# Kernel optimization log

Hardware: AMD Instinct MI355X
Metric: run time of the kernel (lower is better)

Reference implementation:

```python
import jax, jax.numpy as jnp
import numpy as np

TOPK = 8
NUM_EXPERT_GROUP = 8
TOPK_GROUP = 4
ROUTED_SCALING_FACTOR = 2.5

NUM_TOKENS = 131072
NUM_EXPERTS = 256


def setup_inputs() -> dict:
    key = jax.random.key(0)
    k1, k2 = jax.random.split(key)
    router_logits = jax.random.normal(k1, (NUM_TOKENS, NUM_EXPERTS), dtype=jnp.float32)
    correction_bias = jax.random.normal(k2, (NUM_EXPERTS,), dtype=jnp.float32)
    return {"router_logits": router_logits, "correction_bias": correction_bias}


def reference(router_logits, correction_bias):
    # Biased grouped top-k router (DeepSeek-V3 style), faithful to TopK.__call__
    logits = router_logits.astype(jnp.float32)          # [T, E]
    T, E = logits.shape
    G = NUM_EXPERT_GROUP
    experts_per_group = E // G

    scores_for_choice = logits + correction_bias[None, :]            # [T, E]
    scores_grouped = scores_for_choice.reshape(T, G, experts_per_group)
    # group score = sum of top-2 biased scores in each group
    group_scores = jnp.sum(jax.lax.top_k(scores_grouped, k=2)[0], axis=-1)  # [T, G]
    group_idx = jax.lax.top_k(group_scores, k=TOPK_GROUP)[1]                 # [T, KG]
    group_mask = jnp.clip(jax.nn.one_hot(group_idx, G).sum(axis=1), 0, 1)    # [T, G]
    score_mask = jnp.broadcast_to(group_mask[:, :, None], (T, G, experts_per_group)).reshape(T, E)
    tmp_scores = jnp.where(score_mask.astype(bool), scores_for_choice, float("-inf"))
    topk_ids = jax.lax.top_k(tmp_scores, k=TOPK)[1]                          # [T, K]
    # weights are gathered from the UNbiased logits
    topk_weights = jnp.take_along_axis(logits, topk_ids, axis=1)             # [T, K]
    # renormalize + routed scaling factor
    topk_weights = topk_weights / jnp.sum(topk_weights, axis=-1, keepdims=True)
    topk_weights = topk_weights * ROUTED_SCALING_FACTOR
    return topk_weights.astype(jnp.float32), topk_ids
```

## Files before the change

kernel.cpp:

```cpp
#include <hip/hip_runtime.h>
#include <stdint.h>
#include <math.h>

static constexpr int TOPK   = 8;
static constexpr int TOPKG  = 4;
static constexpr int NEXP   = 256;
static constexpr float RSF  = 2.5f;

static constexpr int DPP_QX1 = 0xB1;
static constexpr int DPP_QX2 = 0x4E;
static constexpr int DPP_HM  = 0x141;
static constexpr int DPP_MIR = 0x140;
static constexpr int DPP_B15 = 0x142;
static constexpr int DPP_B31 = 0x143;

template <int CTRL>
__device__ __forceinline__ float dppmov(float x) {
    int xi = __float_as_int(x);
    return __int_as_float(__builtin_amdgcn_update_dpp(xi, xi, CTRL, 0xF, 0xF, false));
}

__device__ __forceinline__ void cas(float& ax, float& ay, int& ix, int& iy) {
    bool p   = ax < ay;
    float hi = fmaxf(ax, ay), lo = fminf(ax, ay);
    int   nx = p ? iy : ix,   ny = p ? ix : iy;
    ax = hi; ay = lo; ix = nx; iy = ny;
}

__global__ __launch_bounds__(256) void router_kernel(
    const float* __restrict__ logits,
    const float* __restrict__ bias,
    float* __restrict__ out_w,
    float* __restrict__ out_id,
    int T)
{
    const int lane  = threadIdx.x & 63;
    const int token = blockIdx.x * (blockDim.x >> 6) + (threadIdx.x >> 6);
    if (token >= T) return;

    const float* row = logits + (size_t)token * NEXP;
    float4 v = ((const float4*)row)[lane];
    float4 b = ((const float4*)bias)[lane];

    float s0 = v.x + b.x;
    float s1 = v.y + b.y;
    float s2 = v.z + b.z;
    float s3 = v.w + b.w;

    float hi01 = fmaxf(s0, s1), lo01 = fminf(s0, s1);
    float hi23 = fmaxf(s2, s3), lo23 = fminf(s2, s3);
    float m1 = fmaxf(hi01, hi23);
    float m2 = fmaxf(fminf(hi01, hi23), fmaxf(lo01, lo23));
    {
        float o1 = dppmov<DPP_QX1>(m1), o2 = dppmov<DPP_QX1>(m2);
        float n1 = fmaxf(m1, o1);
        float n2 = fmaxf(fminf(m1, o1), fmaxf(m2, o2));
        m1 = n1; m2 = n2;
    }
    {
        float o1 = dppmov<DPP_QX2>(m1), o2 = dppmov<DPP_QX2>(m2);
        float n1 = fmaxf(m1, o1);
        float n2 = fmaxf(fminf(m1, o1), fmaxf(m2, o2));
        m1 = n1; m2 = n2;
    }
    {
        float o1 = dppmov<DPP_HM>(m1), o2 = dppmov<DPP_HM>(m2);
        float n1 = fmaxf(m1, o1);
        float n2 = fmaxf(fminf(m1, o1), fmaxf(m2, o2));
        m1 = n1; m2 = n2;
    }
    const float gscore = m1 + m2;

    const int g = lane >> 3;
    const int j = lane & 7;
    float gj = __shfl(gscore, j << 3, 64);
    bool beats = (gj > gscore) || (gj == gscore && j < g);
    uint64_t bal = __ballot(beats);
    int rank = __popcll(bal & (0xFFull << (g << 3)));
    const bool sel = (rank < TOPKG);

    const float NEG = -INFINITY;
    float a0 = sel ? s0 : NEG;
    float a1 = sel ? s1 : NEG;
    float a2 = sel ? s2 : NEG;
    float a3 = sel ? s3 : NEG;
    const int ebase = lane << 2;
    int i0 = ebase, i1 = ebase + 1, i2 = ebase + 2, i3 = ebase + 3;
    cas(a0, a1, i0, i1);
    cas(a2, a3, i2, i3);
    cas(a0, a2, i0, i2);
    cas(a1, a3, i1, i3);
    cas(a1, a2, i1, i2);
    uint32_t ipack = (uint32_t)i0 | ((uint32_t)i1 << 8) |
                     ((uint32_t)i2 << 16) | ((uint32_t)i3 << 24);
    int i0cur = i0;

    int   myid = 0;
    float myw  = 0.f;
    #pragma unroll
    for (int r = 0; r < TOPK; ++r) {
        float x = a0;
        x = fmaxf(x, dppmov<DPP_QX1>(x));
        x = fmaxf(x, dppmov<DPP_QX2>(x));
        x = fmaxf(x, dppmov<DPP_HM >(x));
        x = fmaxf(x, dppmov<DPP_MIR>(x));
        x = fmaxf(x, dppmov<DPP_B15>(x));
        x = fmaxf(x, dppmov<DPP_B31>(x));
        const float smax = __int_as_float(
            __builtin_amdgcn_readlane(__float_as_int(x), 63));

        uint64_t wb  = __ballot(a0 == smax);
        const int wl = __ffsll((unsigned long long)wb) - 1;
        const int idx = __builtin_amdgcn_readlane(i0cur, wl);

        const bool mine = (lane == r);
        myid = mine ? idx  : myid;
        myw  = mine ? smax : myw;

        const bool win = (lane == wl);
        a0 = win ? a1  : a0;
        a1 = win ? a2  : a1;
        a2 = win ? a3  : a2;
        a3 = win ? NEG : a3;
        ipack = win ? (ipack >> 8) : ipack;
        i0cur = (int)(ipack & 255u);
    }

    float bi = 0.f;
    if (lane < TOPK) bi = bias[myid];
    float w = myw - bi;

    float t = w;
    t += dppmov<DPP_QX1>(t);
    t += dppmov<DPP_QX2>(t);
    t += dppmov<DPP_HM >(t);

    if (lane < TOPK) {
        out_w [(size_t)token * TOPK + lane] = w / t * RSF;
        out_id[(size_t)token * TOPK + lane] = (float)myid;
    }
}

extern "C" void kernel_launch(void* const* d_in, const int* in_sizes, int n_in,
                              void* d_out, int out_size, void* d_ws, size_t ws_size,
                              hipStream_t stream) {
    const float* logits = (const float*)d_in[0];
    const float* bias   = (const float*)d_in[1];
    const int T = in_sizes[0] / NEXP;
    float* out = (float*)d_out;
    float* out_w  = out;
    float* out_id = out + (size_t)T * TOPK;

    const int waves_per_block = 256 / 64;
    const int blocks = (T + waves_per_block - 1) / waves_per_block;
    router_kernel<<<blocks, 256, 0, stream>>>(logits, bias, out_w, out_id, T);
}
```

Before: 218.5 us.

## Use sortable uint keys and cached per-row maxima in top-k selection

Biased scores become order-preserving uint32 keys, so comparisons are integer max/select. The top-k loop keeps four cached row maxima (one per 16-lane row) and, after each pick, recomputes only the winner's row with a 4-step DPP reduction instead of a full 6-step wave reduction. The final weights are re-read from the logits row rather than subtracting bias from the stored score. Each round still pays a full row reduction plus a readlane, and re-reading the row adds a global load that will likely hit cache.

```diff
diff --git a/kernel.cpp b/kernel.cpp
--- a/kernel.cpp
+++ b/kernel.cpp
@@ -2,28 +2,35 @@
 #include <stdint.h>
 #include <math.h>
 
-static constexpr int TOPK   = 8;
-static constexpr int TOPKG  = 4;
-static constexpr int NEXP   = 256;
-static constexpr float RSF  = 2.5f;
+static constexpr int TOPK  = 8;
+static constexpr int TOPKG = 4;
+static constexpr int NEXP  = 256;
+static constexpr float RSF = 2.5f;
 
 static constexpr int DPP_QX1 = 0xB1;
 static constexpr int DPP_QX2 = 0x4E;
 static constexpr int DPP_HM  = 0x141;
 static constexpr int DPP_MIR = 0x140;
-static constexpr int DPP_B15 = 0x142;
-static constexpr int DPP_B31 = 0x143;
 
 template <int CTRL>
-__device__ __forceinline__ float dppmov(float x) {
+__device__ __forceinline__ float dppmov_f(float x) {
     int xi = __float_as_int(x);
     return __int_as_float(__builtin_amdgcn_update_dpp(xi, xi, CTRL, 0xF, 0xF, false));
 }
+template <int CTRL>
+__device__ __forceinline__ uint32_t dppmov_u(uint32_t x) {
+    return (uint32_t)__builtin_amdgcn_update_dpp((int)x, (int)x, CTRL, 0xF, 0xF, false);
+}
 
-__device__ __forceinline__ void cas(float& ax, float& ay, int& ix, int& iy) {
-    bool p   = ax < ay;
-    float hi = fmaxf(ax, ay), lo = fminf(ax, ay);
-    int   nx = p ? iy : ix,   ny = p ? ix : iy;
+__device__ __forceinline__ uint32_t f2sort(float f) {
+    uint32_t u = __float_as_uint(f);
+    return u ^ ((uint32_t)((int32_t)u >> 31) | 0x80000000u);
+}
+
+__device__ __forceinline__ void cas(uint32_t& ax, uint32_t& ay, int& ix, int& iy) {
+    bool p      = ax < ay;
+    uint32_t hi = p ? ay : ax, lo = p ? ax : ay;
+    int nx      = p ? iy : ix,  ny = p ? ix : iy;
     ax = hi; ay = lo; ix = nx; iy = ny;
 }
 
@@ -52,19 +59,19 @@
     float m1 = fmaxf(hi01, hi23);
     float m2 = fmaxf(fminf(hi01, hi23), fmaxf(lo01, lo23));
     {
-        float o1 = dppmov<DPP_QX1>(m1), o2 = dppmov<DPP_QX1>(m2);
+        float o1 = dppmov_f<DPP_QX1>(m1), o2 = dppmov_f<DPP_QX1>(m2);
         float n1 = fmaxf(m1, o1);
         float n2 = fmaxf(fminf(m1, o1), fmaxf(m2, o2));
         m1 = n1; m2 = n2;
     }
     {
-        float o1 = dppmov<DPP_QX2>(m1), o2 = dppmov<DPP_QX2>(m2);
+        float o1 = dppmov_f<DPP_QX2>(m1), o2 = dppmov_f<DPP_QX2>(m2);
         float n1 = fmaxf(m1, o1);
         float n2 = fmaxf(fminf(m1, o1), fmaxf(m2, o2));
         m1 = n1; m2 = n2;
     }
     {
-        float o1 = dppmov<DPP_HM>(m1), o2 = dppmov<DPP_HM>(m2);
+        float o1 = dppmov_f<DPP_HM>(m1), o2 = dppmov_f<DPP_HM>(m2);
         float n1 = fmaxf(m1, o1);
         float n2 = fmaxf(fminf(m1, o1), fmaxf(m2, o2));
         m1 = n1; m2 = n2;
@@ -75,15 +82,14 @@
     const int j = lane & 7;
     float gj = __shfl(gscore, j << 3, 64);
     bool beats = (gj > gscore) || (gj == gscore && j < g);
-    uint64_t bal = __ballot(beats);
-    int rank = __popcll(bal & (0xFFull << (g << 3)));
+    uint64_t balg = __ballot(beats);
+    int rank = __popcll(balg & (0xFFull << (g << 3)));
     const bool sel = (rank < TOPKG);
 
-    const float NEG = -INFINITY;
-    float a0 = sel ? s0 : NEG;
-    float a1 = sel ? s1 : NEG;
-    float a2 = sel ? s2 : NEG;
-    float a3 = sel ? s3 : NEG;
+    uint32_t a0 = sel ? f2sort(s0) : 0u;
+    uint32_t a1 = sel ? f2sort(s1) : 0u;
+    uint32_t a2 = sel ? f2sort(s2) : 0u;
+    uint32_t a3 = sel ? f2sort(s3) : 0u;
     const int ebase = lane << 2;
     int i0 = ebase, i1 = ebase + 1, i2 = ebase + 2, i3 = ebase + 3;
     cas(a0, a1, i0, i1);
@@ -93,47 +99,54 @@
     cas(a1, a2, i1, i2);
     uint32_t ipack = (uint32_t)i0 | ((uint32_t)i1 << 8) |
                      ((uint32_t)i2 << 16) | ((uint32_t)i3 << 24);
-    int i0cur = i0;
 
-    int   myid = 0;
-    float myw  = 0.f;
+    uint32_t bm = a0;
+    bm = max(bm, dppmov_u<DPP_QX1>(bm));
+    bm = max(bm, dppmov_u<DPP_QX2>(bm));
+    bm = max(bm, dppmov_u<DPP_HM >(bm));
+    bm = max(bm, dppmov_u<DPP_MIR>(bm));
+    uint32_t rm0 = (uint32_t)__builtin_amdgcn_readlane((int)bm,  0);
+    uint32_t rm1 = (uint32_t)__builtin_amdgcn_readlane((int)bm, 16);
+    uint32_t rm2 = (uint32_t)__builtin_amdgcn_readlane((int)bm, 32);
+    uint32_t rm3 = (uint32_t)__builtin_amdgcn_readlane((int)bm, 48);
+
+    int myid = 0;
     #pragma unroll
     for (int r = 0; r < TOPK; ++r) {
-        float x = a0;
-        x = fmaxf(x, dppmov<DPP_QX1>(x));
-        x = fmaxf(x, dppmov<DPP_QX2>(x));
-        x = fmaxf(x, dppmov<DPP_HM >(x));
-        x = fmaxf(x, dppmov<DPP_MIR>(x));
-        x = fmaxf(x, dppmov<DPP_B15>(x));
-        x = fmaxf(x, dppmov<DPP_B31>(x));
-        const float smax = __int_as_float(
-            __builtin_amdgcn_readlane(__float_as_int(x), 63));
+        const uint32_t smax = max(max(rm0, rm1), max(rm2, rm3));
 
-        uint64_t wb  = __ballot(a0 == smax);
-        const int wl = __ffsll((unsigned long long)wb) - 1;
-        const int idx = __builtin_amdgcn_readlane(i0cur, wl);
+        const uint64_t bal = __ballot(a0 == smax);
+        const int wl  = __ffsll((unsigned long long)bal) - 1;
+        const int idx = __builtin_amdgcn_readlane((int)ipack, wl) & 255;
 
-        const bool mine = (lane == r);
-        myid = mine ? idx  : myid;
-        myw  = mine ? smax : myw;
+        myid = (lane == r) ? idx : myid;
 
         const bool win = (lane == wl);
-        a0 = win ? a1  : a0;
-        a1 = win ? a2  : a1;
-        a2 = win ? a3  : a2;
-        a3 = win ? NEG : a3;
+        a0 = win ? a1 : a0;
+        a1 = win ? a2 : a1;
+        a2 = win ? a3 : a2;
+        a3 = win ? 0u : a3;
         ipack = win ? (ipack >> 8) : ipack;
-        i0cur = (int)(ipack & 255u);
+
+        uint32_t nb = a0;
+        nb = max(nb, dppmov_u<DPP_QX1>(nb));
+        nb = max(nb, dppmov_u<DPP_QX2>(nb));
+        nb = max(nb, dppmov_u<DPP_HM >(nb));
+        nb = max(nb, dppmov_u<DPP_MIR>(nb));
+        const uint32_t nbm = (uint32_t)__builtin_amdgcn_readlane((int)nb, wl);
+        const int blk = wl >> 4;
+        rm0 = (blk == 0) ? nbm : rm0;
+        rm1 = (blk == 1) ? nbm : rm1;
+        rm2 = (blk == 2) ? nbm : rm2;
+        rm3 = (blk == 3) ? nbm : rm3;
     }
 
-    float bi = 0.f;
-    if (lane < TOPK) bi = bias[myid];
-    float w = myw - bi;
-
+    float w = 0.f;
+    if (lane < TOPK) w = row[myid];
     float t = w;
-    t += dppmov<DPP_QX1>(t);
-    t += dppmov<DPP_QX2>(t);
-    t += dppmov<DPP_HM >(t);
+    t += dppmov_f<DPP_QX1>(t);
+    t += dppmov_f<DPP_QX2>(t);
+    t += dppmov_f<DPP_HM >(t);
 
     if (lane < TOPK) {
         out_w [(size_t)token * TOPK + lane] = w / t * RSF;
```

Result: faster. 206.5 us (-5.5%).
